# Performance work log

Measured on AMD Instinct MI355X. Metric: run time of the kernel, lower is better.

Reference implementation:

```python
import jax, jax.numpy as jnp
import numpy as np

B, V, D, H = 128, 32, 64, 256
E = V * (V - 1)  # 992 directed edges (no self loops)
_edges = np.ones((V, V)) - np.eye(V)
SEND, RECV = np.where(_edges)  # each len E


def _mlp(x, w1, b1, w2, b2, w3, b3):
    h = jax.nn.relu(x @ w1.T + b1)
    h = jax.nn.relu(h @ w2.T + b2)
    return h @ w3.T + b3


def setup_inputs() -> dict:
    key = jax.random.key(0)
    ks = iter(jax.random.split(key, 48))
    def w(shape, scale=0.05):
        return jax.random.normal(next(ks), shape, jnp.float32) * scale
    d = {}
    d['inputs'] = jax.random.normal(next(ks), (B, V, D), jnp.float32)
    d['h0'] = jax.random.normal(next(ks), (B, E, H), jnp.float32) * 0.1
    d['c0'] = jax.random.normal(next(ks), (B, E, H), jnp.float32) * 0.1
    for name, ind in (('m1', D), ('m2', 2 * H), ('m3', H), ('m4', 3 * H)):
        d[name + 'w1'] = w((H, ind)); d[name + 'b1'] = jnp.full((H,), 0.1, jnp.float32)
        d[name + 'w2'] = w((H, H));   d[name + 'b2'] = jnp.full((H,), 0.1, jnp.float32)
        d[name + 'w3'] = w((H, H));   d[name + 'b3'] = jnp.full((H,), 0.1, jnp.float32)
    d['wih'] = w((4 * H, H)); d['whh'] = w((4 * H, H))
    d['bih'] = jnp.zeros((4 * H,), jnp.float32); d['bhh'] = jnp.zeros((4 * H,), jnp.float32)
    d['pw1'] = w((H, H)); d['pb1'] = jnp.full((H,), 0.1, jnp.float32)
    d['pw2'] = w((H, H)); d['pb2'] = jnp.full((H,), 0.1, jnp.float32)
    d['pw3'] = w((2, H)); d['pb3'] = jnp.full((2,), 0.1, jnp.float32)
    return d


def reference(inputs, h0, c0,
              m1w1, m1b1, m1w2, m1b2, m1w3, m1b3,
              m2w1, m2b1, m2w2, m2b2, m2w3, m2b3,
              m3w1, m3b1, m3w2, m3b2, m3w3, m3b3,
              m4w1, m4b1, m4w2, m4b2, m4w3, m4b3,
              wih, whh, bih, bhh,
              pw1, pb1, pw2, pb2, pw3, pb3):
    send, recv = jnp.asarray(SEND), jnp.asarray(RECV)
    # edge2node one-hot matrix [V, E] (fixed, non-trainable in original)
    e2n = (recv[None, :] == jnp.arange(V)[:, None]).astype(inputs.dtype)

    x = _mlp(inputs, m1w1, m1b1, m1w2, m1b2, m1w3, m1b3)          # [B,V,H]
    x = jnp.concatenate([x[:, send], x[:, recv]], axis=-1)         # [B,E,2H]
    x = _mlp(x, m2w1, m2b1, m2w2, m2b2, m2w3, m2b3)                # [B,E,H]
    x_skip = x
    x = jnp.einsum('ve,beh->bvh', e2n, x) / (V - 1)                # [B,V,H]
    x = _mlp(x, m3w1, m3b1, m3w2, m3b2, m3w3, m3b3)                # [B,V,H]
    x = jnp.concatenate([x[:, send], x[:, recv], x_skip], axis=-1)  # [B,E,3H]
    x = _mlp(x, m4w1, m4b1, m4w2, m4b2, m4w3, m4b3)                # [B,E,H]

    # single-step LSTM over B*E independent sequences of length 1
    gates = x @ wih.T + bih + h0 @ whh.T + bhh                     # [B,E,4H]
    i, f, g, o = jnp.split(gates, 4, axis=-1)
    c1 = jax.nn.sigmoid(f) * c0 + jax.nn.sigmoid(i) * jnp.tanh(g)
    h1 = jax.nn.sigmoid(o) * jnp.tanh(c1)

    prior_result = _mlp(h1, pw1, pb1, pw2, pb2, pw3, pb3)          # [B,E,2]
    return prior_result, h1, c1
```

## Files before the change

kernel.cpp:

```cpp
#include <hip/hip_runtime.h>
#include <math.h>

#define B_ 128
#define V_ 32
#define D_ 64
#define H_ 256
#define E_ 992
#define ME (B_*E_)
#define MV (B_*V_)

typedef __attribute__((ext_vector_type(8))) short bf8v;
typedef __attribute__((ext_vector_type(4))) float f4v;
typedef __attribute__((ext_vector_type(8))) unsigned short u16x8;

__device__ __forceinline__ unsigned short f2bf(float f) {
    union { float f; unsigned int u; } v; v.f = f;
    unsigned int u = v.u + 0x7FFFu + ((v.u >> 16) & 1u);
    return (unsigned short)(u >> 16);
}
__device__ __forceinline__ float bf2f(unsigned short h) {
    union { unsigned int u; float f; } v; v.u = ((unsigned int)h) << 16;
    return v.f;
}
__device__ __forceinline__ float sigf(float x) {
    x = fminf(fmaxf(x, -30.f), 30.f);
    return 1.f / (1.f + __expf(-x));
}
__device__ __forceinline__ float tanhf_fast(float x) {
    x = fminf(fmaxf(x, -15.f), 15.f);
    float e = __expf(2.f * x);
    return (e - 1.f) / (e + 1.f);
}
__device__ __forceinline__ void gl_lds16(const unsigned short* g, unsigned short* l) {
    __builtin_amdgcn_global_load_lds(
        (const __attribute__((address_space(1))) unsigned int*)g,
        (__attribute__((address_space(3))) unsigned int*)l, 16, 0, 0);
}

__global__ __launch_bounds__(256)
void f2b_k(const float* __restrict__ s, unsigned short* __restrict__ d, int n4)
{
    const int g = blockIdx.x * 256 + threadIdx.x;
    if (g >= n4) return;
    const float4 v = ((const float4*)s)[g];
    ushort4 o;
    o.x = f2bf(v.x); o.y = f2bf(v.y); o.z = f2bf(v.z); o.w = f2bf(v.w);
    ((ushort4*)d)[g] = o;
}

__global__ __launch_bounds__(256)
void f2bs_k(const float* __restrict__ s, unsigned short* __restrict__ d,
            int rows, int cols4, int ld, int off)
{
    const int g = blockIdx.x * 256 + threadIdx.x;
    if (g >= rows * cols4) return;
    const int r = g / cols4, c4 = g - r * cols4;
    const float4 v = *(const float4*)(s + (size_t)r * ld + off + c4 * 4);
    ushort4 o;
    o.x = f2bf(v.x); o.y = f2bf(v.y); o.z = f2bf(v.z); o.w = f2bf(v.w);
    *(ushort4*)(d + (size_t)r * cols4 * 4 + c4 * 4) = o;
}

__global__ __launch_bounds__(256)
void gemm_k(const float* __restrict__ A, int lda,
            const float* __restrict__ W, int ldw,
            const float* __restrict__ bias,
            float* __restrict__ out,
            int M, int N, int K, int do_relu)
{
    __shared__ float As[32][68];
    __shared__ float Ws[32][68];
    const int m0 = blockIdx.x * 64;
    const int n0 = blockIdx.y * 64;
    const int t  = threadIdx.x;
    const int tx = t & 15, ty = t >> 4;
    const int lm = t >> 3;
    const int lk = (t & 7) * 4;

    float acc[4][4] = {};

    for (int k0 = 0; k0 < K; k0 += 32) {
        #pragma unroll
        for (int h = 0; h < 2; ++h) {
            const int m = m0 + lm + h * 32;
            const float4 v = *(const float4*)(A + (size_t)m * lda + k0 + lk);
            As[lk + 0][lm + h * 32] = v.x;
            As[lk + 1][lm + h * 32] = v.y;
            As[lk + 2][lm + h * 32] = v.z;
            As[lk + 3][lm + h * 32] = v.w;
            const int n = n0 + lm + h * 32;
            const float4 w = *(const float4*)(W + (size_t)n * ldw + k0 + lk);
            Ws[lk + 0][lm + h * 32] = w.x;
            Ws[lk + 1][lm + h * 32] = w.y;
            Ws[lk + 2][lm + h * 32] = w.z;
            Ws[lk + 3][lm + h * 32] = w.w;
        }
        __syncthreads();
        #pragma unroll
        for (int kk = 0; kk < 32; ++kk) {
            float a[4], b[4];
            #pragma unroll
            for (int i = 0; i < 4; ++i) a[i] = As[kk][ty * 4 + i];
            #pragma unroll
            for (int j = 0; j < 4; ++j) b[j] = Ws[kk][tx * 4 + j];
            #pragma unroll
            for (int i = 0; i < 4; ++i)
                #pragma unroll
                for (int j = 0; j < 4; ++j)
                    acc[i][j] = fmaf(a[i], b[j], acc[i][j]);
        }
        __syncthreads();
    }

    #pragma unroll
    for (int i = 0; i < 4; ++i) {
        const int m = m0 + ty * 4 + i;
        const size_t ob = (size_t)m * N;
        #pragma unroll
        for (int j = 0; j < 4; ++j) {
            const int n = n0 + tx * 4 + j;
            float v = acc[i][j];
            if (bias) v += bias[n];
            if (do_relu) v = fmaxf(v, 0.f);
            out[ob + n] = v;
        }
    }
}

template<int EPI, int RELU>
__global__ __launch_bounds__(256)
void gemm_mfma(const unsigned short* __restrict__ A, int lda,
               const unsigned short* __restrict__ W,
               const float* __restrict__ bias,
               unsigned short* __restrict__ out,
               const float* __restrict__ ES, const float* __restrict__ ER)
{
    __shared__ alignas(16) unsigned short As[2][4096];
    __shared__ alignas(16) unsigned short Bs[2][4096];
    const int t = threadIdx.x;
    const int lane = t & 63, wid = t >> 6;
    const int wr = wid >> 1, wc = wid & 1;
    const int m0 = blockIdx.x * 128, n0 = blockIdx.y * 128;
    const int srow = t >> 2, scol = (t & 3) * 8;

    f4v acc[4][4];
    #pragma unroll
    for (int i = 0; i < 4; ++i)
        #pragma unroll
        for (int j = 0; j < 4; ++j)
            acc[i][j] = (f4v){0.f, 0.f, 0.f, 0.f};

#define STAGE_G(buf, k0) do { \
    gl_lds16(A + (size_t)(m0 + srow) * lda + (k0) + scol,      &As[buf][t * 8]); \
    gl_lds16(A + (size_t)(m0 + 64 + srow) * lda + (k0) + scol, &As[buf][2048 + t * 8]); \
    gl_lds16(W + (size_t)(n0 + srow) * 256 + (k0) + scol,      &Bs[buf][t * 8]); \
    gl_lds16(W + (size_t)(n0 + 64 + srow) * 256 + (k0) + scol, &Bs[buf][2048 + t * 8]); \
} while (0)

    STAGE_G(0, 0);
    __syncthreads();
    int cur = 0;
    #pragma unroll
    for (int s = 0; s < 8; ++s) {
        if (s < 7) STAGE_G(cur ^ 1, (s + 1) * 32);
        const unsigned short* Ab = As[cur];
        const unsigned short* Bb = Bs[cur];
        const int kof = (lane >> 4) * 8;
        const int rA = wr * 64 + (lane & 15);
        const int rB = wc * 64 + (lane & 15);
        bf8v af[4], bv[4];
        #pragma unroll
        for (int f = 0; f < 4; ++f) af[f] = *(const bf8v*)&Ab[(rA + f * 16) * 32 + kof];
        #pragma unroll
        for (int f = 0; f < 4; ++f) bv[f] = *(const bf8v*)&Bb[(rB + f * 16) * 32 + kof];
        #pragma unroll
        for (int i = 0; i < 4; ++i)
            #pragma unroll
            for (int j = 0; j < 4; ++j)
                acc[i][j] = __builtin_amdgcn_mfma_f32_16x16x32_bf16(af[i], bv[j], acc[i][j], 0, 0, 0);
        __syncthreads();
        cur ^= 1;
    }
#undef STAGE_G

    #pragma unroll
    for (int i = 0; i < 4; ++i) {
        #pragma unroll
        for (int r = 0; r < 4; ++r) {
            const int m = m0 + wr * 64 + i * 16 + (lane >> 4) * 4 + r;
            size_t bs = 0, br = 0;
            if (EPI) {
                const int bb = m / E_;
                const int e  = m - bb * E_;
                const int sS = e / 31;
                const int jj = e - sS * 31;
                const int rr = jj + (jj >= sS ? 1 : 0);
                bs = ((size_t)bb * V_ + sS) * H_;
                br = ((size_t)bb * V_ + rr) * H_;
            }
            const size_t ob = (size_t)m * 256;
            #pragma unroll
            for (int j = 0; j < 4; ++j) {
                const int n = n0 + wc * 64 + j * 16 + (lane & 15);
                float v = acc[i][j][r] + bias[n];
                if (EPI) v += ES[bs + n] + ER[br + n];
                if (RELU) v = fmaxf(v, 0.f);
                out[ob + n] = f2bf(v);
            }
        }
    }
}

__global__ __launch_bounds__(256)
void lstm_mfma(const unsigned short* __restrict__ x4b, const unsigned short* __restrict__ h0b,
               const float* __restrict__ c0,
               const unsigned short* __restrict__ wihb, const unsigned short* __restrict__ whhb,
               const float* __restrict__ bih, const float* __restrict__ bhh,
               float* __restrict__ h1, float* __restrict__ c1,
               unsigned short* __restrict__ h1b)
{
    __shared__ alignas(16) unsigned short As[2][4096];
    __shared__ alignas(16) unsigned short Bs[2][4096];
    const int t = threadIdx.x;
    const int lane = t & 63, wid = t >> 6;
    const int wr = wid >> 1, wc = wid & 1;
    const int m0 = blockIdx.x * 128;
    const int jb = blockIdx.y * 32;
    const int srow = t >> 2, scol = (t & 3) * 8;
    const int rl0 = srow, rl1 = srow + 64;
    const size_t wrow0 = (size_t)((rl0 >> 5) * 256 + jb + (rl0 & 31)) * 256;
    const size_t wrow1 = (size_t)((rl1 >> 5) * 256 + jb + (rl1 & 31)) * 256;

    f4v acc[4][4];
    #pragma unroll
    for (int i = 0; i < 4; ++i)
        #pragma unroll
        for (int j = 0; j < 4; ++j)
            acc[i][j] = (f4v){0.f, 0.f, 0.f, 0.f};

#define STAGE_L(buf, s) do { \
    const int k0_ = (s) * 32; \
    const unsigned short* Ap_ = (k0_ < 256) ? x4b : h0b; \
    const unsigned short* Wp_ = (k0_ < 256) ? wihb : whhb; \
    const int kk_ = k0_ & 255; \
    gl_lds16(Ap_ + (size_t)(m0 + srow) * 256 + kk_ + scol,      &As[buf][t * 8]); \
    gl_lds16(Ap_ + (size_t)(m0 + 64 + srow) * 256 + kk_ + scol, &As[buf][2048 + t * 8]); \
    gl_lds16(Wp_ + wrow0 + kk_ + scol, &Bs[buf][t * 8]); \
    gl_lds16(Wp_ + wrow1 + kk_ + scol, &Bs[buf][2048 + t * 8]); \
} while (0)

    STAGE_L(0, 0);
    __syncthreads();
    int cur = 0;
    #pragma unroll
    for (int s = 0; s < 16; ++s) {
        if (s < 15) STAGE_L(cur ^ 1, s + 1);
        const unsigned short* Ab = As[cur];
        const unsigned short* Bb = Bs[cur];
        const int kof = (lane >> 4) * 8;
        const int rA = wr * 64 + (lane & 15);
        bf8v af[4], bg[4];
        #pragma unroll
        for (int f = 0; f < 4; ++f) af[f] = *(const bf8v*)&Ab[(rA + f * 16) * 32 + kof];
        #pragma unroll
        for (int g = 0; g < 4; ++g) bg[g] = *(const bf8v*)&Bb[(g * 32 + wc * 16 + (lane & 15)) * 32 + kof];
        #pragma unroll
        for (int i = 0; i < 4; ++i)
            #pragma unroll
            for (int g = 0; g < 4; ++g)
                acc[i][g] = __builtin_amdgcn_mfma_f32_16x16x32_bf16(af[i], bg[g], acc[i][g], 0, 0, 0);
        __syncthreads();
        cur ^= 1;
    }
#undef STAGE_L

    const int j = jb + wc * 16 + (lane & 15);
    const float bi0 = bih[j] + bhh[j];
    const float bi1 = bih[256 + j] + bhh[256 + j];
    const float bi2 = bih[512 + j] + bhh[512 + j];
    const float bi3 = bih[768 + j] + bhh[768 + j];
    #pragma unroll
    for (int i = 0; i < 4; ++i) {
        #pragma unroll
        for (int r = 0; r < 4; ++r) {
            const int row = m0 + wr * 64 + i * 16 + (lane >> 4) * 4 + r;
            const size_t o = (size_t)row * 256 + j;
            const float gi = acc[i][0][r] + bi0;
            const float gf = acc[i][1][r] + bi1;
            const float gg = acc[i][2][r] + bi2;
            const float go = acc[i][3][r] + bi3;
            const float cn = sigf(gf) * c0[o] + sigf(gi) * tanhf_fast(gg);
            const float hn = sigf(go) * tanhf_fast(cn);
            c1[o] = cn;
            h1[o] = hn;
            h1b[o] = f2bf(hn);
        }
    }
}

__global__ __launch_bounds__(256)
void edge_l1_k(const float* __restrict__ Ys, const float* __restrict__ Yr,
               const float* __restrict__ bias, unsigned short* __restrict__ out)
{
    const int g = blockIdx.x * 256 + threadIdx.x;
    const int n4  = (g & 63) * 4;
    const int row = g >> 6;
    const int b = row / E_;
    const int e = row - b * E_;
    const int s = e / 31;
    const int jj = e - s * 31;
    const int r = jj + (jj >= s ? 1 : 0);
    const float4 ys = *(const float4*)(Ys + ((size_t)b * V_ + s) * H_ + n4);
    const float4 yr = *(const float4*)(Yr + ((size_t)b * V_ + r) * H_ + n4);
    const float4 bv = *(const float4*)(bias + n4);
    ushort4 o;
    o.x = f2bf(fmaxf(ys.x + yr.x + bv.x, 0.f));
    o.y = f2bf(fmaxf(ys.y + yr.y + bv.y, 0.f));
    o.z = f2bf(fmaxf(ys.z + yr.z + bv.z, 0.f));
    o.w = f2bf(fmaxf(ys.w + yr.w + bv.w, 0.f));
    *(ushort4*)(out + (size_t)row * 256 + n4) = o;
}

__global__ __launch_bounds__(256)
void agg_k(const unsigned short* __restrict__ X2, float* __restrict__ outv)
{
    const int g = blockIdx.x * 256 + threadIdx.x;
    const int h = g & 255;
    const int v = (g >> 8) & 31;
    const int b = g >> 13;
    float s = 0.f;
    #pragma unroll
    for (int snd = 0; snd < 32; ++snd) {
        if (snd == v) continue;
        const int e = snd * 31 + v - (snd < v ? 1 : 0);
        s += bf2f(X2[((size_t)b * E_ + e) * H_ + h]);
    }
    outv[g] = s * (1.f / 31.f);
}

__global__ __launch_bounds__(256)
void prior3_k(const unsigned short* __restrict__ Hin, const float* __restrict__ w,
              const float* __restrict__ bias, float* __restrict__ out)
{
    const int t   = threadIdx.x;
    const int row = blockIdx.x * 16 + (t >> 4);
    const int kb  = (t & 15) * 16;
    const unsigned short* a = Hin + (size_t)row * 256 + kb;
    const u16x8 a0 = *(const u16x8*)a;
    const u16x8 a1 = *(const u16x8*)(a + 8);
    float p0 = 0.f, p1 = 0.f;
    #pragma unroll
    for (int i = 0; i < 8; ++i) {
        const float x0 = bf2f(a0[i]), x1 = bf2f(a1[i]);
        p0 += x0 * w[kb + i] + x1 * w[kb + 8 + i];
        p1 += x0 * w[256 + kb + i] + x1 * w[256 + kb + 8 + i];
    }
    #pragma unroll
    for (int off = 8; off >= 1; off >>= 1) {
        p0 += __shfl_xor(p0, off, 16);
        p1 += __shfl_xor(p1, off, 16);
    }
    if ((t & 15) == 0) {
        out[(size_t)row * 2 + 0] = p0 + bias[0];
        out[(size_t)row * 2 + 1] = p1 + bias[1];
    }
}

extern "C" void kernel_launch(void* const* d_in, const int* in_sizes, int n_in,
                              void* d_out, int out_size, void* d_ws, size_t ws_size,
                              hipStream_t stream)
{
    const float* inputs = (const float*)d_in[0];
    const float* h0     = (const float*)d_in[1];
    const float* c0     = (const float*)d_in[2];
    const float* m1w1 = (const float*)d_in[3];  const float* m1b1 = (const float*)d_in[4];
    const float* m1w2 = (const float*)d_in[5];  const float* m1b2 = (const float*)d_in[6];
    const float* m1w3 = (const float*)d_in[7];  const float* m1b3 = (const float*)d_in[8];
    const float* m2w1 = (const float*)d_in[9];  const float* m2b1 = (const float*)d_in[10];
    const float* m2w2 = (const float*)d_in[11]; const float* m2b2 = (const float*)d_in[12];
    const float* m2w3 = (const float*)d_in[13]; const float* m2b3 = (const float*)d_in[14];
    const float* m3w1 = (const float*)d_in[15]; const float* m3b1 = (const float*)d_in[16];
    const float* m3w2 = (const float*)d_in[17]; const float* m3b2 = (const float*)d_in[18];
    const float* m3w3 = (const float*)d_in[19]; const float* m3b3 = (const float*)d_in[20];
    const float* m4w1 = (const float*)d_in[21]; const float* m4b1 = (const float*)d_in[22];
    const float* m4w2 = (const float*)d_in[23]; const float* m4b2 = (const float*)d_in[24];
    const float* m4w3 = (const float*)d_in[25]; const float* m4b3 = (const float*)d_in[26];
    const float* wih  = (const float*)d_in[27]; const float* whh  = (const float*)d_in[28];
    const float* bih  = (const float*)d_in[29]; const float* bhh  = (const float*)d_in[30];
    const float* pw1  = (const float*)d_in[31]; const float* pb1  = (const float*)d_in[32];
    const float* pw2  = (const float*)d_in[33]; const float* pb2  = (const float*)d_in[34];
    const float* pw3  = (const float*)d_in[35]; const float* pb3  = (const float*)d_in[36];

    float* out   = (float*)d_out;
    float* prior = out;
    float* h1    = out + (size_t)ME * 2;
    float* c1    = h1 + (size_t)ME * H_;

    float* S0 = (float*)d_ws;
    float* S1 = S0 + (size_t)MV * H_;
    float* S2 = S1 + (size_t)MV * H_;
    float* S3 = S2 + (size_t)MV * H_;
    unsigned short* EA = (unsigned short*)(S3 + (size_t)MV * H_);
    unsigned short* EB = EA + (size_t)ME * H_;
    unsigned short* EC = EB + (size_t)ME * H_;
    unsigned short* cw22 = EC + (size_t)ME * H_;
    unsigned short* cw23 = cw22 + 65536;
    unsigned short* cw41 = cw23 + 65536;
    unsigned short* cw42 = cw41 + 65536;
    unsigned short* cw43 = cw42 + 65536;
    unsigned short* cpw1 = cw43 + 65536;
    unsigned short* cpw2 = cpw1 + 65536;
    unsigned short* cwih = cpw2 + 65536;
    unsigned short* cwhh = cwih + 262144;

    const dim3 blk(256);
    const dim3 gV(MV / 64, 4);
    const dim3 gM(ME / 128, 2);

    f2b_k<<<64, blk, 0, stream>>>(m2w2, cw22, 16384);
    f2b_k<<<64, blk, 0, stream>>>(m2w3, cw23, 16384);
    f2bs_k<<<64, blk, 0, stream>>>(m4w1, cw41, 256, 64, 768, 512);
    f2b_k<<<64, blk, 0, stream>>>(m4w2, cw42, 16384);
    f2b_k<<<64, blk, 0, stream>>>(m4w3, cw43, 16384);
    f2b_k<<<64, blk, 0, stream>>>(pw1, cpw1, 16384);
    f2b_k<<<64, blk, 0, stream>>>(pw2, cpw2, 16384);
    f2b_k<<<256, blk, 0, stream>>>(wih, cwih, 65536);
    f2b_k<<<256, blk, 0, stream>>>(whh, cwhh, 65536);
    f2b_k<<<ME * H_ / 1024, blk, 0, stream>>>(h0, EC, ME * H_ / 4);

    gemm_k<<<gV, blk, 0, stream>>>(inputs, 64, m1w1, 64, m1b1, S0, MV, 256, 64, 1);
    gemm_k<<<gV, blk, 0, stream>>>(S0, 256, m1w2, 256, m1b2, S1, MV, 256, 256, 1);
    gemm_k<<<gV, blk, 0, stream>>>(S1, 256, m1w3, 256, m1b3, S0, MV, 256, 256, 0);

    gemm_k<<<gV, blk, 0, stream>>>(S0, 256, m2w1,       512, nullptr, S2, MV, 256, 256, 0);
    gemm_k<<<gV, blk, 0, stream>>>(S0, 256, m2w1 + 256, 512, nullptr, S3, MV, 256, 256, 0);

    edge_l1_k<<<ME * 64 / 256, blk, 0, stream>>>(S2, S3, m2b1, EA);
    gemm_mfma<0, 1><<<gM, blk, 0, stream>>>(EA, 256, cw22, m2b2, EB, nullptr, nullptr);
    gemm_mfma<0, 0><<<gM, blk, 0, stream>>>(EB, 256, cw23, m2b3, EA, nullptr, nullptr);

    agg_k<<<MV * H_ / 256, blk, 0, stream>>>(EA, S0);
    gemm_k<<<gV, blk, 0, stream>>>(S0, 256, m3w1, 256, m3b1, S1, MV, 256, 256, 1);
    gemm_k<<<gV, blk, 0, stream>>>(S1, 256, m3w2, 256, m3b2, S0, MV, 256, 256, 1);
    gemm_k<<<gV, blk, 0, stream>>>(S0, 256, m3w3, 256, m3b3, S1, MV, 256, 256, 0);

    gemm_k<<<gV, blk, 0, stream>>>(S1, 256, m4w1,       768, nullptr, S2, MV, 256, 256, 0);
    gemm_k<<<gV, blk, 0, stream>>>(S1, 256, m4w1 + 256, 768, nullptr, S3, MV, 256, 256, 0);

    gemm_mfma<1, 1><<<gM, blk, 0, stream>>>(EA, 256, cw41, m4b1, EB, S2, S3);
    gemm_mfma<0, 1><<<gM, blk, 0, stream>>>(EB, 256, cw42, m4b2, EA, nullptr, nullptr);
    gemm_mfma<0, 0><<<gM, blk, 0, stream>>>(EA, 256, cw43, m4b3, EB, nullptr, nullptr);

    lstm_mfma<<<dim3(ME / 128, 8), blk, 0, stream>>>(EB, EC, c0, cwih, cwhh, bih, bhh, h1, c1, EA);

    gemm_mfma<0, 1><<<gM, blk, 0, stream>>>(EA, 256, cpw1, pb1, EB, nullptr, nullptr);
    gemm_mfma<0, 1><<<gM, blk, 0, stream>>>(EB, 256, cpw2, pb2, EC, nullptr, nullptr);
    prior3_k<<<ME / 16, blk, 0, stream>>>(EC, pw3, pb3, prior);
}
```

Before: 1.331 ms.

## Fuse edge MLP chains, LSTM and prior into LDS-resident per-tile kernels

Measured after the change: 1.382 ms. 1.04x slower.

```diff
diff --git a/kernel.cpp b/kernel.cpp
--- a/kernel.cpp
+++ b/kernel.cpp
@@ -35,6 +35,10 @@
     __builtin_amdgcn_global_load_lds(
         (const __attribute__((address_space(1))) unsigned int*)g,
         (__attribute__((address_space(3))) unsigned int*)l, 16, 0, 0);
+}
+
+__device__ __forceinline__ int tidx(int row, int k) {
+    return row * 256 + (k ^ ((row & 7) << 3));
 }
 
 __global__ __launch_bounds__(256)
@@ -127,21 +131,17 @@
     }
 }
 
-template<int EPI, int RELU>
-__global__ __launch_bounds__(256)
-void gemm_mfma(const unsigned short* __restrict__ A, int lda,
-               const unsigned short* __restrict__ W,
-               const float* __restrict__ bias,
-               unsigned short* __restrict__ out,
-               const float* __restrict__ ES, const float* __restrict__ ER)
-{
-    __shared__ alignas(16) unsigned short As[2][4096];
-    __shared__ alignas(16) unsigned short Bs[2][4096];
-    const int t = threadIdx.x;
-    const int lane = t & 63, wid = t >> 6;
-    const int wr = wid >> 1, wc = wid & 1;
-    const int m0 = blockIdx.x * 128, n0 = blockIdx.y * 128;
-    const int srow = t >> 2, scol = (t & 3) * 8;
+template<int RELU, int EPI>
+__device__ __forceinline__ void chain_gemm(
+    unsigned short* T, unsigned short* Wst,
+    const unsigned short* __restrict__ W, const float* __restrict__ bias,
+    int m0, const float* __restrict__ ES, const float* __restrict__ ER)
+{
+    const int t = threadIdx.x, lane = t & 63, wid = t >> 6;
+    const int r = wid >> 2, c = wid & 3;
+    const int kof = (lane >> 4) * 8;
+    const int ra = r * 64 + (lane & 15);
+    const int q1 = t & 255, kp1 = t >> 8;
 
     f4v acc[4][4];
     #pragma unroll
@@ -150,46 +150,45 @@
         for (int j = 0; j < 4; ++j)
             acc[i][j] = (f4v){0.f, 0.f, 0.f, 0.f};
 
-#define STAGE_G(buf, k0) do { \
-    gl_lds16(A + (size_t)(m0 + srow) * lda + (k0) + scol,      &As[buf][t * 8]); \
-    gl_lds16(A + (size_t)(m0 + 64 + srow) * lda + (k0) + scol, &As[buf][2048 + t * 8]); \
-    gl_lds16(W + (size_t)(n0 + srow) * 256 + (k0) + scol,      &Bs[buf][t * 8]); \
-    gl_lds16(W + (size_t)(n0 + 64 + srow) * 256 + (k0) + scol, &Bs[buf][2048 + t * 8]); \
-} while (0)
-
-    STAGE_G(0, 0);
+    gl_lds16(W + (size_t)q1 * 256 + kp1 * 8,       Wst + t * 8);
+    gl_lds16(W + (size_t)q1 * 256 + (kp1 + 2) * 8, Wst + 4096 + t * 8);
     __syncthreads();
     int cur = 0;
     #pragma unroll
     for (int s = 0; s < 8; ++s) {
-        if (s < 7) STAGE_G(cur ^ 1, (s + 1) * 32);
-        const unsigned short* Ab = As[cur];
-        const unsigned short* Bb = Bs[cur];
-        const int kof = (lane >> 4) * 8;
-        const int rA = wr * 64 + (lane & 15);
-        const int rB = wc * 64 + (lane & 15);
-        bf8v af[4], bv[4];
-        #pragma unroll
-        for (int f = 0; f < 4; ++f) af[f] = *(const bf8v*)&Ab[(rA + f * 16) * 32 + kof];
-        #pragma unroll
-        for (int f = 0; f < 4; ++f) bv[f] = *(const bf8v*)&Bb[(rB + f * 16) * 32 + kof];
+        if (s < 7) {
+            const int k0 = (s + 1) * 32;
+            gl_lds16(W + (size_t)q1 * 256 + k0 + kp1 * 8,       Wst + (cur ^ 1) * 8192 + t * 8);
+            gl_lds16(W + (size_t)q1 * 256 + k0 + (kp1 + 2) * 8, Wst + (cur ^ 1) * 8192 + 4096 + t * 8);
+        }
+        bf8v a[4], b[4];
+        #pragma unroll
+        for (int f = 0; f < 4; ++f) {
+            const int rr = ra + f * 16;
+            a[f] = *(const bf8v*)&T[tidx(rr, s * 32 + kof)];
+            b[f] = *(const bf8v*)&Wst[cur * 8192 + (lane >> 4) * 2048 + (c * 64 + f * 16 + (lane & 15)) * 8];
+        }
         #pragma unroll
         for (int i = 0; i < 4; ++i)
             #pragma unroll
             for (int j = 0; j < 4; ++j)
-                acc[i][j] = __builtin_amdgcn_mfma_f32_16x16x32_bf16(af[i], bv[j], acc[i][j], 0, 0, 0);
+                acc[i][j] = __builtin_amdgcn_mfma_f32_16x16x32_bf16(a[i], b[j], acc[i][j], 0, 0, 0);
         __syncthreads();
         cur ^= 1;
     }
-#undef STAGE_G
-
-    #pragma unroll
-    for (int i = 0; i < 4; ++i) {
-        #pragma unroll
-        for (int r = 0; r < 4; ++r) {
-            const int m = m0 + wr * 64 + i * 16 + (lane >> 4) * 4 + r;
+
+    float bv[4];
+    #pragma unroll
+    for (int nf = 0; nf < 4; ++nf) bv[nf] = bias[c * 64 + nf * 16 + (lane & 15)];
+
+    #pragma unroll
+    for (int mf = 0; mf < 4; ++mf) {
+        #pragma unroll
+        for (int reg = 0; reg < 4; ++reg) {
+            const int row = r * 64 + mf * 16 + (lane >> 4) * 4 + reg;
             size_t bs = 0, br = 0;
             if (EPI) {
+                const int m  = m0 + row;
                 const int bb = m / E_;
                 const int e  = m - bb * E_;
                 const int sS = e / 31;
@@ -198,38 +197,82 @@
                 bs = ((size_t)bb * V_ + sS) * H_;
                 br = ((size_t)bb * V_ + rr) * H_;
             }
-            const size_t ob = (size_t)m * 256;
             #pragma unroll
-            for (int j = 0; j < 4; ++j) {
-                const int n = n0 + wc * 64 + j * 16 + (lane & 15);
-                float v = acc[i][j][r] + bias[n];
+            for (int nf = 0; nf < 4; ++nf) {
+                const int n = c * 64 + nf * 16 + (lane & 15);
+                float v = acc[mf][nf][reg] + bv[nf];
                 if (EPI) v += ES[bs + n] + ER[br + n];
                 if (RELU) v = fmaxf(v, 0.f);
-                out[ob + n] = f2bf(v);
+                T[tidx(row, n)] = f2bf(v);
             }
         }
     }
-}
-
-__global__ __launch_bounds__(256)
-void lstm_mfma(const unsigned short* __restrict__ x4b, const unsigned short* __restrict__ h0b,
-               const float* __restrict__ c0,
-               const unsigned short* __restrict__ wihb, const unsigned short* __restrict__ whhb,
-               const float* __restrict__ bih, const float* __restrict__ bhh,
-               float* __restrict__ h1, float* __restrict__ c1,
-               unsigned short* __restrict__ h1b)
-{
-    __shared__ alignas(16) unsigned short As[2][4096];
-    __shared__ alignas(16) unsigned short Bs[2][4096];
-    const int t = threadIdx.x;
-    const int lane = t & 63, wid = t >> 6;
-    const int wr = wid >> 1, wc = wid & 1;
+    __syncthreads();
+}
+
+__global__ __launch_bounds__(512, 2)
+void chain1_k(const float* __restrict__ Ys, const float* __restrict__ Yr,
+              const float* __restrict__ b1,
+              const unsigned short* __restrict__ w2, const float* __restrict__ b2,
+              const unsigned short* __restrict__ w3, const float* __restrict__ b3,
+              unsigned short* __restrict__ X2out)
+{
+    __shared__ alignas(16) unsigned short T[32768];
+    __shared__ alignas(16) unsigned short Wst[16384];
+    const int t  = threadIdx.x;
     const int m0 = blockIdx.x * 128;
-    const int jb = blockIdx.y * 32;
-    const int srow = t >> 2, scol = (t & 3) * 8;
-    const int rl0 = srow, rl1 = srow + 64;
-    const size_t wrow0 = (size_t)((rl0 >> 5) * 256 + jb + (rl0 & 31)) * 256;
-    const size_t wrow1 = (size_t)((rl1 >> 5) * 256 + jb + (rl1 & 31)) * 256;
+
+    #pragma unroll
+    for (int it = 0; it < 16; ++it) {
+        const int q   = it * 512 + t;
+        const int row = q >> 6;
+        const int n4  = (q & 63) * 4;
+        const int m  = m0 + row;
+        const int bb = m / E_;
+        const int e  = m - bb * E_;
+        const int s  = e / 31;
+        const int jj = e - s * 31;
+        const int rv = jj + (jj >= s ? 1 : 0);
+        const float4 ys = *(const float4*)&Ys[((size_t)bb * V_ + s)  * H_ + n4];
+        const float4 yr = *(const float4*)&Yr[((size_t)bb * V_ + rv) * H_ + n4];
+        const float4 bx = *(const float4*)&b1[n4];
+        ushort4 o;
+        o.x = f2bf(fmaxf(ys.x + yr.x + bx.x, 0.f));
+        o.y = f2bf(fmaxf(ys.y + yr.y + bx.y, 0.f));
+        o.z = f2bf(fmaxf(ys.z + yr.z + bx.z, 0.f));
+        o.w = f2bf(fmaxf(ys.w + yr.w + bx.w, 0.f));
+        *(ushort4*)&T[tidx(row, n4)] = o;
+    }
+    __syncthreads();
+
+    chain_gemm<1, 0>(T, Wst, w2, b2, m0, nullptr, nullptr);
+    chain_gemm<0, 0>(T, Wst, w3, b3, m0, nullptr, nullptr);
+
+    #pragma unroll
+    for (int it = 0; it < 8; ++it) {
+        const int g   = it * 512 + t;
+        const int row = g >> 5;
+        const int kp  = (g & 31) * 8;
+        *(u16x8*)&X2out[(size_t)(m0 + row) * 256 + kp] = *(const u16x8*)&T[tidx(row, kp)];
+    }
+}
+
+__device__ __forceinline__ void lstm_pass(
+    const unsigned short* T, unsigned short* Wst, unsigned short* Ast,
+    const unsigned short* __restrict__ h0b,
+    const unsigned short* __restrict__ wih, const unsigned short* __restrict__ whh,
+    const float* __restrict__ bih, const float* __restrict__ bhh,
+    const float* __restrict__ c0,
+    float* __restrict__ h1, float* __restrict__ c1, unsigned short* __restrict__ h1b,
+    int m0, int jc)
+{
+    const int t = threadIdx.x, lane = t & 63, wid = t >> 6;
+    const int r = wid >> 2, c = wid & 3;
+    const int kof = (lane >> 4) * 8;
+    const int ra = r * 64 + (lane & 15);
+    const int q1 = t & 255, kp1 = t >> 8;
+    const size_t grow = (size_t)((q1 >> 6) * 256 + jc * 64 + (q1 & 63)) * 256;
+    const int qa = t & 127, kpa = t >> 7;
 
     f4v acc[4][4];
     #pragma unroll
@@ -238,57 +281,55 @@
         for (int j = 0; j < 4; ++j)
             acc[i][j] = (f4v){0.f, 0.f, 0.f, 0.f};
 
-#define STAGE_L(buf, s) do { \
-    const int k0_ = (s) * 32; \
-    const unsigned short* Ap_ = (k0_ < 256) ? x4b : h0b; \
-    const unsigned short* Wp_ = (k0_ < 256) ? wihb : whhb; \
-    const int kk_ = k0_ & 255; \
-    gl_lds16(Ap_ + (size_t)(m0 + srow) * 256 + kk_ + scol,      &As[buf][t * 8]); \
-    gl_lds16(Ap_ + (size_t)(m0 + 64 + srow) * 256 + kk_ + scol, &As[buf][2048 + t * 8]); \
-    gl_lds16(Wp_ + wrow0 + kk_ + scol, &Bs[buf][t * 8]); \
-    gl_lds16(Wp_ + wrow1 + kk_ + scol, &Bs[buf][2048 + t * 8]); \
-} while (0)
-
-    STAGE_L(0, 0);
+    gl_lds16(wih + grow + kp1 * 8,       Wst + t * 8);
+    gl_lds16(wih + grow + (kp1 + 2) * 8, Wst + 4096 + t * 8);
     __syncthreads();
     int cur = 0;
     #pragma unroll
     for (int s = 0; s < 16; ++s) {
-        if (s < 15) STAGE_L(cur ^ 1, s + 1);
-        const unsigned short* Ab = As[cur];
-        const unsigned short* Bb = Bs[cur];
-        const int kof = (lane >> 4) * 8;
-        const int rA = wr * 64 + (lane & 15);
-        bf8v af[4], bg[4];
-        #pragma unroll
-        for (int f = 0; f < 4; ++f) af[f] = *(const bf8v*)&Ab[(rA + f * 16) * 32 + kof];
-        #pragma unroll
-        for (int g = 0; g < 4; ++g) bg[g] = *(const bf8v*)&Bb[(g * 32 + wc * 16 + (lane & 15)) * 32 + kof];
+        if (s < 15) {
+            const int s2 = s + 1;
+            const unsigned short* Wm = (s2 < 8) ? wih : whh;
+            const int k0 = (s2 & 7) * 32;
+            gl_lds16(Wm + grow + k0 + kp1 * 8,       Wst + (cur ^ 1) * 8192 + t * 8);
+            gl_lds16(Wm + grow + k0 + (kp1 + 2) * 8, Wst + (cur ^ 1) * 8192 + 4096 + t * 8);
+            if (s2 >= 8) {
+                const int ka = (s2 - 8) * 32;
+                gl_lds16(h0b + (size_t)(m0 + qa) * 256 + ka + kpa * 8, Ast + (cur ^ 1) * 4096 + t * 8);
+            }
+        }
+        bf8v a[4], b[4];
+        #pragma unroll
+        for (int f = 0; f < 4; ++f) {
+            const int rr = ra + f * 16;
+            if (s < 8) a[f] = *(const bf8v*)&T[tidx(rr, s * 32 + kof)];
+            else       a[f] = *(const bf8v*)&Ast[cur * 4096 + (lane >> 4) * 1024 + rr * 8];
+            b[f] = *(const bf8v*)&Wst[cur * 8192 + (lane >> 4) * 2048 + (f * 64 + c * 16 + (lane & 15)) * 8];
+        }
         #pragma unroll
         for (int i = 0; i < 4; ++i)
             #pragma unroll
             for (int g = 0; g < 4; ++g)
-                acc[i][g] = __builtin_amdgcn_mfma_f32_16x16x32_bf16(af[i], bg[g], acc[i][g], 0, 0, 0);
+                acc[i][g] = __builtin_amdgcn_mfma_f32_16x16x32_bf16(a[i], b[g], acc[i][g], 0, 0, 0);
         __syncthreads();
         cur ^= 1;
     }
-#undef STAGE_L
-
-    const int j = jb + wc * 16 + (lane & 15);
-    const float bi0 = bih[j] + bhh[j];
+
+    const int j = jc * 64 + c * 16 + (lane & 15);
+    const float bi0 = bih[j]       + bhh[j];
     const float bi1 = bih[256 + j] + bhh[256 + j];
     const float bi2 = bih[512 + j] + bhh[512 + j];
     const float bi3 = bih[768 + j] + bhh[768 + j];
     #pragma unroll
-    for (int i = 0; i < 4; ++i) {
-        #pragma unroll
-        for (int r = 0; r < 4; ++r) {
-            const int row = m0 + wr * 64 + i * 16 + (lane >> 4) * 4 + r;
-            const size_t o = (size_t)row * 256 + j;
-            const float gi = acc[i][0][r] + bi0;
-            const float gf = acc[i][1][r] + bi1;
-            const float gg = acc[i][2][r] + bi2;
-            const float go = acc[i][3][r] + bi3;
+    for (int mf = 0; mf < 4; ++mf) {
+        #pragma unroll
+        for (int reg = 0; reg < 4; ++reg) {
+            const int row = r * 64 + mf * 16 + (lane >> 4) * 4 + reg;
+            const size_t o = (size_t)(m0 + row) * 256 + j;
+            const float gi = acc[mf][0][reg] + bi0;
+            const float gf = acc[mf][1][reg] + bi1;
+            const float gg = acc[mf][2][reg] + bi2;
+            const float go = acc[mf][3][reg] + bi3;
             const float cn = sigf(gf) * c0[o] + sigf(gi) * tanhf_fast(gg);
             const float hn = sigf(go) * tanhf_fast(cn);
             c1[o] = cn;
@@ -296,29 +337,89 @@
             h1b[o] = f2bf(hn);
         }
     }
-}
-
-__global__ __launch_bounds__(256)
-void edge_l1_k(const float* __restrict__ Ys, const float* __restrict__ Yr,
-               const float* __restrict__ bias, unsigned short* __restrict__ out)
-{
-    const int g = blockIdx.x * 256 + threadIdx.x;
-    const int n4  = (g & 63) * 4;
-    const int row = g >> 6;
-    const int b = row / E_;
-    const int e = row - b * E_;
-    const int s = e / 31;
-    const int jj = e - s * 31;
-    const int r = jj + (jj >= s ? 1 : 0);
-    const float4 ys = *(const float4*)(Ys + ((size_t)b * V_ + s) * H_ + n4);
-    const float4 yr = *(const float4*)(Yr + ((size_t)b * V_ + r) * H_ + n4);
-    const float4 bv = *(const float4*)(bias + n4);
-    ushort4 o;
-    o.x = f2bf(fmaxf(ys.x + yr.x + bv.x, 0.f));
-    o.y = f2bf(fmaxf(ys.y + yr.y + bv.y, 0.f));
-    o.z = f2bf(fmaxf(ys.z + yr.z + bv.z, 0.f));
-    o.w = f2bf(fmaxf(ys.w + yr.w + bv.w, 0.f));
-    *(ushort4*)(out + (size_t)row * 256 + n4) = o;
+    __syncthreads();
+}
+
+__global__ __launch_bounds__(512, 2)
+void chain2_k(const unsigned short* __restrict__ X2,
+              const unsigned short* __restrict__ w41, const float* __restrict__ b41,
+              const unsigned short* __restrict__ w42, const float* __restrict__ b42,
+              const unsigned short* __restrict__ w43, const float* __restrict__ b43,
+              const float* __restrict__ ZS, const float* __restrict__ ZR,
+              const unsigned short* __restrict__ h0b,
+              const unsigned short* __restrict__ wih, const unsigned short* __restrict__ whh,
+              const float* __restrict__ bih, const float* __restrict__ bhh,
+              const float* __restrict__ c0,
+              float* __restrict__ h1, float* __restrict__ c1,
+              unsigned short* __restrict__ h1b)
+{
+    __shared__ alignas(16) unsigned short T[32768];
+    __shared__ alignas(16) unsigned short Wst[16384];
+    __shared__ alignas(16) unsigned short Ast[8192];
+    const int t  = threadIdx.x;
+    const int m0 = blockIdx.x * 128;
+
+    #pragma unroll
+    for (int it = 0; it < 8; ++it) {
+        const int g   = it * 512 + t;
+        const int row = g >> 5;
+        const int kp  = (g & 31) * 8;
+        *(u16x8*)&T[tidx(row, kp)] = *(const u16x8*)&X2[(size_t)(m0 + row) * 256 + kp];
+    }
+    __syncthreads();
+
+    chain_gemm<1, 1>(T, Wst, w41, b41, m0, ZS, ZR);
+    chain_gemm<1, 0>(T, Wst, w42, b42, m0, nullptr, nullptr);
+    chain_gemm<0, 0>(T, Wst, w43, b43, m0, nullptr, nullptr);
+
+    for (int jc = 0; jc < 4; ++jc)
+        lstm_pass(T, Wst, Ast, h0b, wih, whh, bih, bhh, c0, h1, c1, h1b, m0, jc);
+}
+
+__global__ __launch_bounds__(512, 2)
+void prior_k(const unsigned short* __restrict__ Hin,
+             const unsigned short* __restrict__ w1, const float* __restrict__ b1,
+             const unsigned short* __restrict__ w2, const float* __restrict__ b2,
+             const float* __restrict__ w3, const float* __restrict__ b3,
+             float* __restrict__ out)
+{
+    __shared__ alignas(16) unsigned short T[32768];
+    __shared__ alignas(16) unsigned short Wst[16384];
+    const int t  = threadIdx.x;
+    const int m0 = blockIdx.x * 128;
+
+    #pragma unroll
+    for (int it = 0; it < 8; ++it) {
+        const int g   = it * 512 + t;
+        const int row = g >> 5;
+        const int kp  = (g & 31) * 8;
+        *(u16x8*)&T[tidx(row, kp)] = *(const u16x8*)&Hin[(size_t)(m0 + row) * 256 + kp];
+    }
+    __syncthreads();
+
+    chain_gemm<1, 0>(T, Wst, w1, b1, m0, nullptr, nullptr);
+    chain_gemm<1, 0>(T, Wst, w2, b2, m0, nullptr, nullptr);
+
+    const int row = t >> 2;
+    const int kb  = (t & 3) * 64;
+    float p0 = 0.f, p1 = 0.f;
+    #pragma unroll
+    for (int g = 0; g < 8; ++g) {
+        const int k = kb + g * 8;
+        const u16x8 v = *(const u16x8*)&T[tidx(row, k)];
+        #pragma unroll
+        for (int i = 0; i < 8; ++i) {
+            const float x = bf2f(v[i]);
+            p0 += x * w3[k + i];
+            p1 += x * w3[256 + k + i];
+        }
+    }
+    p0 += __shfl_xor(p0, 1); p0 += __shfl_xor(p0, 2);
+    p1 += __shfl_xor(p1, 1); p1 += __shfl_xor(p1, 2);
+    if ((t & 3) == 0) {
+        out[(size_t)(m0 + row) * 2 + 0] = p0 + b3[0];
+        out[(size_t)(m0 + row) * 2 + 1] = p1 + b3[1];
+    }
 }
 
 __global__ __launch_bounds__(256)
@@ -336,34 +437,6 @@
         s += bf2f(X2[((size_t)b * E_ + e) * H_ + h]);
     }
     outv[g] = s * (1.f / 31.f);
-}
-
-__global__ __launch_bounds__(256)
-void prior3_k(const unsigned short* __restrict__ Hin, const float* __restrict__ w,
-              const float* __restrict__ bias, float* __restrict__ out)
-{
-    const int t   = threadIdx.x;
-    const int row = blockIdx.x * 16 + (t >> 4);
-    const int kb  = (t & 15) * 16;
-    const unsigned short* a = Hin + (size_t)row * 256 + kb;
-    const u16x8 a0 = *(const u16x8*)a;
-    const u16x8 a1 = *(const u16x8*)(a + 8);
-    float p0 = 0.f, p1 = 0.f;
-    #pragma unroll
-    for (int i = 0; i < 8; ++i) {
-        const float x0 = bf2f(a0[i]), x1 = bf2f(a1[i]);
-        p0 += x0 * w[kb + i] + x1 * w[kb + 8 + i];
-        p1 += x0 * w[256 + kb + i] + x1 * w[256 + kb + 8 + i];
-    }
-    #pragma unroll
-    for (int off = 8; off >= 1; off >>= 1) {
-        p0 += __shfl_xor(p0, off, 16);
-        p1 += __shfl_xor(p1, off, 16);
-    }
-    if ((t & 15) == 0) {
-        out[(size_t)row * 2 + 0] = p0 + bias[0];
-        out[(size_t)row * 2 + 1] = p1 + bias[1];
-    }
 }
 
 extern "C" void kernel_launch(void* const* d_in, const int* in_sizes, int n_in,
@@ -414,8 +487,9 @@
     unsigned short* cwhh = cwih + 262144;
 
     const dim3 blk(256);
+    const dim3 blk5(512);
     const dim3 gV(MV / 64, 4);
-    const dim3 gM(ME / 128, 2);
+    const dim3 gC(ME / 128);
 
     f2b_k<<<64, blk, 0, stream>>>(m2w2, cw22, 16384);
     f2b_k<<<64, blk, 0, stream>>>(m2w3, cw23, 16384);
@@ -426,7 +500,7 @@
     f2b_k<<<64, blk, 0, stream>>>(pw2, cpw2, 16384);
     f2b_k<<<256, blk, 0, stream>>>(wih, cwih, 65536);
     f2b_k<<<256, blk, 0, stream>>>(whh, cwhh, 65536);
-    f2b_k<<<ME * H_ / 1024, blk, 0, stream>>>(h0, EC, ME * H_ / 4);
+    f2b_k<<<ME * H_ / 1024, blk, 0, stream>>>(h0, EB, ME * H_ / 4);
 
     gemm_k<<<gV, blk, 0, stream>>>(inputs, 64, m1w1, 64, m1b1, S0, MV, 256, 64, 1);
     gemm_k<<<gV, blk, 0, stream>>>(S0, 256, m1w2, 256, m1b2, S1, MV, 256, 256, 1);
@@ -435,9 +509,7 @@
     gemm_k<<<gV, blk, 0, stream>>>(S0, 256, m2w1,       512, nullptr, S2, MV, 256, 256, 0);
     gemm_k<<<gV, blk, 0, stream>>>(S0, 256, m2w1 + 256, 512, nullptr, S3, MV, 256, 256, 0);
 
-    edge_l1_k<<<ME * 64 / 256, blk, 0, stream>>>(S2, S3, m2b1, EA);
-    gemm_mfma<0, 1><<<gM, blk, 0, stream>>>(EA, 256, cw22, m2b2, EB, nullptr, nullptr);
-    gemm_mfma<0, 0><<<gM, blk, 0, stream>>>(EB, 256, cw23, m2b3, EA, nullptr, nullptr);
+    chain1_k<<<gC, blk5, 0, stream>>>(S2, S3, m2b1, cw22, m2b2, cw23, m2b3, EA);
 
     agg_k<<<MV * H_ / 256, blk, 0, stream>>>(EA, S0);
     gemm_k<<<gV, blk, 0, stream>>>(S0, 256, m3w1, 256, m3b1, S1, MV, 256, 256, 1);
@@ -447,13 +519,8 @@
     gemm_k<<<gV, blk, 0, stream>>>(S1, 256, m4w1,       768, nullptr, S2, MV, 256, 256, 0);
     gemm_k<<<gV, blk, 0, stream>>>(S1, 256, m4w1 + 256, 768, nullptr, S3, MV, 256, 256, 0);
 
-    gemm_mfma<1, 1><<<gM, blk, 0, stream>>>(EA, 256, cw41, m4b1, EB, S2, S3);
-    gemm_mfma<0, 1><<<gM, blk, 0, stream>>>(EB, 256, cw42, m4b2, EA, nullptr, nullptr);
-    gemm_mfma<0, 0><<<gM, blk, 0, stream>>>(EA, 256, cw43, m4b3, EB, nullptr, nullptr);
-
-    lstm_mfma<<<dim3(ME / 128, 8), blk, 0, stream>>>(EB, EC, c0, cwih, cwhh, bih, bhh, h1, c1, EA);
-
-    gemm_mfma<0, 1><<<gM, blk, 0, stream>>>(EA, 256, cpw1, pb1, EB, nullptr, nullptr);
-    gemm_mfma<0, 1><<<gM, blk, 0, stream>>>(EB, 256, cpw2, pb2, EC, nullptr, nullptr);
-    prior3_k<<<ME / 16, blk, 0, stream>>>(EC, pw3, pb3, prior);
-}
+    chain2_k<<<gC, blk5, 0, stream>>>(EA, cw41, m4b1, cw42, m4b2, cw43, m4b3,
+                                      S2, S3, EB, cwih, cwhh, bih, bhh, c0, h1, c1, EC);
+
+    prior_k<<<gC, blk5, 0, stream>>>(EC, cpw1, pb1, cpw2, pb2, pw3, pb3, prior);
+}
```
